# Kernel optimization log

Hardware: AMD Instinct MI355X
Metric: run time of the kernel (lower is better)

## Reference

```python
import jax, jax.numpy as jnp
import numpy as np

WINDOW = 48
RES = 50
PRED = 96

def setup_inputs() -> dict:
    key = jax.random.key(0)
    k1, k2, k3, k4, k5 = jax.random.split(key, 5)
    x = jax.random.normal(k1, (2048, 4800, 1), dtype=jnp.float32)
    W_lin = jax.random.normal(k2, (WINDOW, WINDOW), dtype=jnp.float32) * 0.1
    # W_in = inv(P) @ B with P orthogonal, B ~ U(-1,1); statistically a dense random matrix
    W_in = jax.random.uniform(k3, (RES, WINDOW), dtype=jnp.float32, minval=-1.0, maxval=1.0)
    # diagonal reservoir weights d ~ U(-0.95, 0.95)
    d = jax.random.uniform(k4, (RES,), dtype=jnp.float32, minval=-0.95, maxval=0.95)
    W_out = jax.random.normal(k5, (PRED, RES), dtype=jnp.float32) * 0.1
    return {"x": x, "W_lin": W_lin, "W_in": W_in, "d": d, "W_out": W_out}

def reference(x, W_lin, W_in, d, W_out):
    B, S, C = x.shape  # C == 1 (non-individual path requires squeeze(1))
    seg = S // WINDOW
    # permute(0,2,1) -> view(B, C, seg, WINDOW) -> squeeze(1)
    u = x[..., 0].reshape(B, seg, WINDOW)
    # input linear (no bias): u @ W_lin.T
    u = jnp.einsum('bsw,vw->bsv', u, W_lin)
    # input projection into reservoir: W_in @ u_t for every step (one big GEMM)
    v = jnp.einsum('bsw,rw->bsr', u, W_in)  # [B, seg, RES]
    # ESN state persists across the batch loop too (never reset in update_state),
    # so the recurrence is one serial chain over B*seg steps.
    v_flat = v.reshape(B * seg, RES)
    def step(state, vt):
        # activation is LeakyReLU(negative_slope=1.0) == identity
        new = vt + d * state
        return new, new
    _, states = jax.lax.scan(step, jnp.zeros((RES,), dtype=v.dtype), v_flat)
    states = states.reshape(B, seg, RES)
    last = states[:, -1, :]              # [B, RES]
    out = last @ W_out.T                 # [B, PRED]
    return out[:, :, None]               # unsqueeze(1).permute(0,2,1) -> [B, PRED, 1]
```

## Files before the change

kernel.cpp:

```cpp
#include <hip/hip_runtime.h>

#define WINDOW 48
#define RES 50
#define PRED 96
#define BATCH 2048
#define KTOT 4800
#define KTRUNC 12
#define KS 10
#define KRB 512
#define ASTR 516

typedef __attribute__((ext_vector_type(8))) short short8v;
typedef __attribute__((ext_vector_type(4))) float f32x4;
typedef __attribute__((ext_vector_type(4))) int i32x4;
typedef __attribute__((address_space(3))) void lds_void;
typedef const __attribute__((address_space(1))) void gmem_void;

#define OFF_M  0
#define OFF_DJ 2400
#define OFF_DK 8800
#define OFF_WT 9600
#define OFF_KS 14400
#define OFF_LP 178240
#define OFF_L  1202240

__device__ __forceinline__ float ipow(float b, int n) {
    float r = 1.f, p = b;
    while (n) { if (n & 1) r *= p; p *= p; n >>= 1; }
    return r;
}

__device__ __forceinline__ unsigned pack2bf(float v0, float v1) {
    unsigned u0 = __builtin_bit_cast(unsigned, v0);
    unsigned u1 = __builtin_bit_cast(unsigned, v1);
    unsigned t0 = u0 + 0x7FFFu + ((u0 >> 16) & 1u);
    unsigned t1 = u1 + 0x7FFFu + ((u1 >> 16) & 1u);
    return (t0 >> 16) | (t1 & 0xFFFF0000u);
}

__global__ __launch_bounds__(256) void k0a(const float* __restrict__ W_lin,
                                           const float* __restrict__ W_in,
                                           const float* __restrict__ d,
                                           const float* __restrict__ W_out,
                                           float* __restrict__ ws) {
    int f = blockIdx.x * 256 + threadIdx.x;
    if (f < 2400) {
        int r = f / WINDOW, w = f % WINDOW;
        float a0 = 0.f, a1 = 0.f;
#pragma unroll
        for (int v = 0; v < WINDOW; v += 2) {
            a0 = fmaf(W_in[r * WINDOW + v],     W_lin[v * WINDOW + w],       a0);
            a1 = fmaf(W_in[r * WINDOW + v + 1], W_lin[(v + 1) * WINDOW + w], a1);
        }
        ws[OFF_M + f] = a0 + a1;
    } else if (f < 8800) {
        int e = f - 2400;
        int j = e >> 6, r = e & 63;
        ws[OFF_DJ + e] = (r < RES) ? ipow(d[r], 99 - j) : 0.f;
    } else if (f < 9600) {
        int e = f - 8800;
        int k = e / RES, r = e % RES;
        ws[OFF_DK + e] = ipow(ipow(d[r], 100), k);
    } else if (f < 14400) {
        int e = f - 9600;
        int r = e / PRED, o = e % PRED;
        ws[OFF_WT + e] = W_out[o * RES + r];
    }
}

__global__ __launch_bounds__(256) void k0b(const float* __restrict__ ws_c,
                                           float* __restrict__ ws) {
    unsigned idx = blockIdx.x * 256 + threadIdx.x;
    int j = idx & 7;
    int l = (idx >> 3) & 63;
    int n = (idx >> 9) & 3;
    int K = idx >> 11;
    int c = n * 16 + (l & 15);
    int k = K * 32 + ((l >> 4) << 3) + j;
    float val = 0.f;
    if (c < RES && k < KTOT) {
        int jj = k / WINDOW, w = k - jj * WINDOW;
        val = ws_c[OFF_DJ + (jj << 6) + c] * ws_c[OFF_M + c * WINDOW + w];
    }
    unsigned u = __builtin_bit_cast(unsigned, val);
    ((unsigned short*)(ws + OFF_KS))[idx] =
        (unsigned short)((u + 0x7FFFu + ((u >> 16) & 1u)) >> 16);
}

__global__ __launch_bounds__(256, 3) void k1(const float* __restrict__ x,
                                             const float* __restrict__ ws,
                                             float* __restrict__ lp) {
    __shared__ float S[16 * ASTR];
    const unsigned short* KbSw = (const unsigned short*)(ws + OFF_KS);
    int bid = blockIdx.x;
    int mt = bid / KS, ks = bid - mt * KS;
    int b0 = mt * 16, kb = ks * KRB;
    int t = threadIdx.x, w = t >> 6, l = t & 63;
    int row16 = l & 15, kq = l >> 4;

#pragma unroll
    for (int i = 0; i < 8; ++i) {
        int e = t + i * 256;
        int row = e >> 7, q = e & 127;
        const float* gp = x + (size_t)(b0 + row) * KTOT + kb + 4 * q;
        if (kb + 4 * q >= KTOT) gp = x;
        __builtin_amdgcn_global_load_lds((gmem_void*)gp,
                                         (lds_void*)&S[row * ASTR + 4 * q], 16, 0, 0);
    }

    int K0 = ks * 16 + w * 4;
    const unsigned short* bbase = KbSw + (size_t)K0 * 2048 + l * 8;
    short8v B0[4], B1[4], B2[4], B3[4];
#pragma unroll
    for (int st = 0; st < 4; ++st) {
        B0[st] = *(const short8v*)(bbase + st * 2048);
        B1[st] = *(const short8v*)(bbase + st * 2048 + 512);
        B2[st] = *(const short8v*)(bbase + st * 2048 + 1024);
        B3[st] = *(const short8v*)(bbase + st * 2048 + 1536);
    }
    __syncthreads();

    f32x4 acc0 = (f32x4)(0.f), acc1 = (f32x4)(0.f), acc2 = (f32x4)(0.f), acc3 = (f32x4)(0.f);
    const float* abase = S + row16 * ASTR + w * 128 + kq * 8;
#pragma unroll
    for (int st = 0; st < 4; ++st) {
        f32x4 a0 = *(const f32x4*)(abase + st * 32);
        f32x4 a1 = *(const f32x4*)(abase + st * 32 + 4);
        i32x4 wv;
        wv[0] = (int)pack2bf(a0[0], a0[1]);
        wv[1] = (int)pack2bf(a0[2], a0[3]);
        wv[2] = (int)pack2bf(a1[0], a1[1]);
        wv[3] = (int)pack2bf(a1[2], a1[3]);
        short8v av = __builtin_bit_cast(short8v, wv);
        acc0 = __builtin_amdgcn_mfma_f32_16x16x32_bf16(av, B0[st], acc0, 0, 0, 0);
        acc1 = __builtin_amdgcn_mfma_f32_16x16x32_bf16(av, B1[st], acc1, 0, 0, 0);
        acc2 = __builtin_amdgcn_mfma_f32_16x16x32_bf16(av, B2[st], acc2, 0, 0, 0);
        acc3 = __builtin_amdgcn_mfma_f32_16x16x32_bf16(av, B3[st], acc3, 0, 0, 0);
    }
    __syncthreads();

    float* Ps = S + w * 1088;
#pragma unroll
    for (int i = 0; i < 4; ++i) {
        int rr = (kq * 4 + i) * 68;
        Ps[rr + row16]      = acc0[i];
        Ps[rr + row16 + 16] = acc1[i];
        Ps[rr + row16 + 32] = acc2[i];
        Ps[rr + row16 + 48] = acc3[i];
    }
    __syncthreads();
#pragma unroll
    for (int i = 0; i < 4; ++i) {
        int o = t + i * 256;
        int r = o >> 6, c = o & 63;
        if (c < RES) {
            float sum = (S[r * 68 + c] + S[1088 + r * 68 + c])
                      + (S[2176 + r * 68 + c] + S[3264 + r * 68 + c]);
            lp[((size_t)ks * BATCH + b0 + r) * 50 + c] = sum;
        }
    }
}

__global__ __launch_bounds__(256) void k2a(float* __restrict__ ws) {
    int e = blockIdx.x * 256 + threadIdx.x;
    const f32x4* lp4 = (const f32x4*)(ws + OFF_LP);
    f32x4 sum = lp4[e];
#pragma unroll
    for (int sp = 1; sp < KS; ++sp)
        sum += lp4[(size_t)sp * 25600 + e];
    ((f32x4*)(ws + OFF_L))[e] = sum;
}

__global__ __launch_bounds__(256) void k2b(const float* __restrict__ ws,
                                           float* __restrict__ out) {
    const float* L  = ws + OFF_L;
    const float* Dk = ws + OFF_DK;
    const float* Wt = ws + OFF_WT;
    __shared__ float s_s[4][52];
    int B0 = blockIdx.x * 4;
    int t = threadIdx.x;
    if (t < 200) {
        int i = t / 50, r = t - (t / 50) * 50;
        int b = B0 + i;
        float acc = 0.f;
#pragma unroll
        for (int k = 0; k < KTRUNC; ++k) {
            int bb = b - k;
            if (bb >= 0) acc = fmaf(Dk[k * RES + r], L[(size_t)bb * 50 + r], acc);
        }
        s_s[i][r] = acc;
    }
    __syncthreads();
#pragma unroll
    for (int o = t; o < 4 * PRED; o += 256) {
        int i = o / PRED, oo = o - (o / PRED) * PRED;
        float acc = 0.f;
#pragma unroll 10
        for (int r = 0; r < RES; ++r)
            acc = fmaf(s_s[i][r], Wt[r * PRED + oo], acc);
        out[(B0 + i) * PRED + oo] = acc;
    }
}

extern "C" void kernel_launch(void* const* d_in, const int* in_sizes, int n_in,
                              void* d_out, int out_size, void* d_ws, size_t ws_size,
                              hipStream_t stream) {
    const float* x     = (const float*)d_in[0];
    const float* W_lin = (const float*)d_in[1];
    const float* W_in  = (const float*)d_in[2];
    const float* d     = (const float*)d_in[3];
    const float* W_out = (const float*)d_in[4];
    float* out = (float*)d_out;
    float* ws  = (float*)d_ws;
    float* lp  = ws + OFF_LP;

    k0a<<<57, 256, 0, stream>>>(W_lin, W_in, d, W_out, ws);
    k0b<<<1280, 256, 0, stream>>>(ws, ws);
    k1<<<128 * KS, 256, 0, stream>>>(x, ws, lp);
    k2a<<<100, 256, 0, stream>>>(ws);
    k2b<<<512, 256, 0, stream>>>(ws, out);
}
```

Baseline: 32.96 us.

## Split GEMM into bf16 pre-swizzle pass and LDS-free MFMA kernel

The x operand is now converted to bf16 in a separate kernel and stored in a swizzled, MFMA-fragment-ready layout in workspace. The GEMM kernel then loads A fragments straight from global memory, with no LDS staging and no in-loop conversion. The aim is to cut LDS traffic and conversion work in the main kernel and raise occupancy. In exchange it adds a kernel launch plus an extra write and read of a bf16 copy of x (about 20 MB) through global memory.

```diff
diff --git a/kernel.cpp b/kernel.cpp
--- a/kernel.cpp
+++ b/kernel.cpp
@@ -7,22 +7,19 @@
 #define KTOT 4800
 #define KTRUNC 12
 #define KS 10
-#define KRB 512
-#define ASTR 516
 
 typedef __attribute__((ext_vector_type(8))) short short8v;
 typedef __attribute__((ext_vector_type(4))) float f32x4;
 typedef __attribute__((ext_vector_type(4))) int i32x4;
-typedef __attribute__((address_space(3))) void lds_void;
-typedef const __attribute__((address_space(1))) void gmem_void;
 
 #define OFF_M  0
 #define OFF_DJ 2400
 #define OFF_DK 8800
 #define OFF_WT 9600
 #define OFF_KS 14400
-#define OFF_LP 178240
-#define OFF_L  1202240
+#define OFF_XB 178240
+#define OFF_LP 5421120
+#define OFF_L  6445120
 
 __device__ __forceinline__ float ipow(float b, int n) {
     float r = 1.f, p = b;
@@ -87,66 +84,73 @@
         (unsigned short)((u + 0x7FFFu + ((u >> 16) & 1u)) >> 16);
 }
 
-__global__ __launch_bounds__(256, 3) void k1(const float* __restrict__ x,
-                                             const float* __restrict__ ws,
-                                             float* __restrict__ lp) {
-    __shared__ float S[16 * ASTR];
+__global__ __launch_bounds__(256) void k1a(const float* __restrict__ x,
+                                           float* __restrict__ ws) {
+    __shared__ float Xs[16 * 132];
+    int bid = blockIdx.x;
+    int mt = bid / 40, kg = bid - mt * 40;
+    int t = threadIdx.x;
+    int kbase = kg * 128;
+#pragma unroll
+    for (int i = 0; i < 2; ++i) {
+        int idx = t + i * 256;
+        int row = idx >> 5, q = idx & 31;
+        int gk = kbase + q * 4;
+        f32x4 v = (f32x4)(0.f);
+        if (gk < KTOT)
+            v = *(const f32x4*)(x + (size_t)(mt * 16 + row) * KTOT + gk);
+        *(f32x4*)(&Xs[row * 132 + q * 4]) = v;
+    }
+    __syncthreads();
+    int K = t >> 6, l = t & 63;
+    int row = l & 15, kq = l >> 4;
+    const float* s = &Xs[row * 132 + K * 32 + kq * 8];
+    i32x4 o;
+    o[0] = (int)pack2bf(s[0], s[1]);
+    o[1] = (int)pack2bf(s[2], s[3]);
+    o[2] = (int)pack2bf(s[4], s[5]);
+    o[3] = (int)pack2bf(s[6], s[7]);
+    unsigned short* Xb = (unsigned short*)(ws + OFF_XB);
+    *(i32x4*)(Xb + ((size_t)(mt * 160 + kg * 4 + K) * 64 + l) * 8) = o;
+}
+
+__global__ __launch_bounds__(256, 4) void k1b(const float* __restrict__ ws,
+                                              float* __restrict__ lp) {
+    __shared__ float Ps[4 * 16 * 68];
     const unsigned short* KbSw = (const unsigned short*)(ws + OFF_KS);
+    const unsigned short* Xb   = (const unsigned short*)(ws + OFF_XB);
     int bid = blockIdx.x;
     int mt = bid / KS, ks = bid - mt * KS;
-    int b0 = mt * 16, kb = ks * KRB;
+    int b0 = mt * 16;
     int t = threadIdx.x, w = t >> 6, l = t & 63;
     int row16 = l & 15, kq = l >> 4;
 
-#pragma unroll
-    for (int i = 0; i < 8; ++i) {
-        int e = t + i * 256;
-        int row = e >> 7, q = e & 127;
-        const float* gp = x + (size_t)(b0 + row) * KTOT + kb + 4 * q;
-        if (kb + 4 * q >= KTOT) gp = x;
-        __builtin_amdgcn_global_load_lds((gmem_void*)gp,
-                                         (lds_void*)&S[row * ASTR + 4 * q], 16, 0, 0);
-    }
-
     int K0 = ks * 16 + w * 4;
+    const unsigned short* abase = Xb + ((size_t)(mt * 160 + K0) * 64 + l) * 8;
     const unsigned short* bbase = KbSw + (size_t)K0 * 2048 + l * 8;
-    short8v B0[4], B1[4], B2[4], B3[4];
+
+    f32x4 acc0 = (f32x4)(0.f), acc1 = (f32x4)(0.f), acc2 = (f32x4)(0.f), acc3 = (f32x4)(0.f);
 #pragma unroll
     for (int st = 0; st < 4; ++st) {
-        B0[st] = *(const short8v*)(bbase + st * 2048);
-        B1[st] = *(const short8v*)(bbase + st * 2048 + 512);
-        B2[st] = *(const short8v*)(bbase + st * 2048 + 1024);
-        B3[st] = *(const short8v*)(bbase + st * 2048 + 1536);
-    }
-    __syncthreads();
-
-    f32x4 acc0 = (f32x4)(0.f), acc1 = (f32x4)(0.f), acc2 = (f32x4)(0.f), acc3 = (f32x4)(0.f);
-    const float* abase = S + row16 * ASTR + w * 128 + kq * 8;
-#pragma unroll
-    for (int st = 0; st < 4; ++st) {
-        f32x4 a0 = *(const f32x4*)(abase + st * 32);
-        f32x4 a1 = *(const f32x4*)(abase + st * 32 + 4);
-        i32x4 wv;
-        wv[0] = (int)pack2bf(a0[0], a0[1]);
-        wv[1] = (int)pack2bf(a0[2], a0[3]);
-        wv[2] = (int)pack2bf(a1[0], a1[1]);
-        wv[3] = (int)pack2bf(a1[2], a1[3]);
-        short8v av = __builtin_bit_cast(short8v, wv);
-        acc0 = __builtin_amdgcn_mfma_f32_16x16x32_bf16(av, B0[st], acc0, 0, 0, 0);
-        acc1 = __builtin_amdgcn_mfma_f32_16x16x32_bf16(av, B1[st], acc1, 0, 0, 0);
-        acc2 = __builtin_amdgcn_mfma_f32_16x16x32_bf16(av, B2[st], acc2, 0, 0, 0);
-        acc3 = __builtin_amdgcn_mfma_f32_16x16x32_bf16(av, B3[st], acc3, 0, 0, 0);
-    }
-    __syncthreads();
-
-    float* Ps = S + w * 1088;
+        short8v av = *(const short8v*)(abase + st * 512);
+        short8v B0 = *(const short8v*)(bbase + st * 2048);
+        short8v B1 = *(const short8v*)(bbase + st * 2048 + 512);
+        short8v B2 = *(const short8v*)(bbase + st * 2048 + 1024);
+        short8v B3 = *(const short8v*)(bbase + st * 2048 + 1536);
+        acc0 = __builtin_amdgcn_mfma_f32_16x16x32_bf16(av, B0, acc0, 0, 0, 0);
+        acc1 = __builtin_amdgcn_mfma_f32_16x16x32_bf16(av, B1, acc1, 0, 0, 0);
+        acc2 = __builtin_amdgcn_mfma_f32_16x16x32_bf16(av, B2, acc2, 0, 0, 0);
+        acc3 = __builtin_amdgcn_mfma_f32_16x16x32_bf16(av, B3, acc3, 0, 0, 0);
+    }
+
+    float* P = Ps + w * 1088;
 #pragma unroll
     for (int i = 0; i < 4; ++i) {
         int rr = (kq * 4 + i) * 68;
-        Ps[rr + row16]      = acc0[i];
-        Ps[rr + row16 + 16] = acc1[i];
-        Ps[rr + row16 + 32] = acc2[i];
-        Ps[rr + row16 + 48] = acc3[i];
+        P[rr + row16]      = acc0[i];
+        P[rr + row16 + 16] = acc1[i];
+        P[rr + row16 + 32] = acc2[i];
+        P[rr + row16 + 48] = acc3[i];
     }
     __syncthreads();
 #pragma unroll
@@ -154,8 +158,8 @@
         int o = t + i * 256;
         int r = o >> 6, c = o & 63;
         if (c < RES) {
-            float sum = (S[r * 68 + c] + S[1088 + r * 68 + c])
-                      + (S[2176 + r * 68 + c] + S[3264 + r * 68 + c]);
+            float sum = (Ps[r * 68 + c] + Ps[1088 + r * 68 + c])
+                      + (Ps[2176 + r * 68 + c] + Ps[3264 + r * 68 + c]);
             lp[((size_t)ks * BATCH + b0 + r) * 50 + c] = sum;
         }
     }
@@ -216,7 +220,8 @@
 
     k0a<<<57, 256, 0, stream>>>(W_lin, W_in, d, W_out, ws);
     k0b<<<1280, 256, 0, stream>>>(ws, ws);
-    k1<<<128 * KS, 256, 0, stream>>>(x, ws, lp);
+    k1a<<<128 * 40, 256, 0, stream>>>(x, ws);
+    k1b<<<128 * KS, 256, 0, stream>>>(ws, lp);
     k2a<<<100, 256, 0, stream>>>(ws);
     k2b<<<512, 256, 0, stream>>>(ws, out);
 }
```

After: 40.31 us. 22.3% more time.
